# Kernel tuning notes

Measured on AMD Instinct MI355X. Metric: run time of the kernel, lower is better.

Reference implementation:

```python
import jax, jax.numpy as jnp
import numpy as np

D_MODEL = 768
N_HEADS = 12
D_HEAD = D_MODEL // N_HEADS

def setup_inputs() -> dict:
    key = jax.random.key(0)
    ks = jax.random.split(key, 5)
    B, T = 2, 4096
    x = jax.random.normal(ks[0], (B, T, D_MODEL), dtype=jnp.float32)
    s_in = 1.0 / np.sqrt(D_MODEL)
    W_qkv = jax.random.normal(ks[1], (D_MODEL, 3 * D_MODEL), dtype=jnp.float32) * s_in
    b_qkv = jnp.zeros((3 * D_MODEL,), dtype=jnp.float32)
    W_proj = jax.random.normal(ks[2], (D_MODEL, D_MODEL), dtype=jnp.float32) * s_in
    b_proj = jnp.zeros((D_MODEL,), dtype=jnp.float32)
    return {"x": x, "W_qkv": W_qkv, "b_qkv": b_qkv, "W_proj": W_proj, "b_proj": b_proj}

def reference(x, W_qkv, b_qkv, W_proj, b_proj):
    B, T, C = x.shape
    qkv = x @ W_qkv + b_qkv                      # [B,T,3C]
    q, k, v = jnp.split(qkv, 3, axis=-1)
    def heads(t):
        return t.reshape(B, T, N_HEADS, D_HEAD).transpose(0, 2, 1, 3)  # [B,H,T,d]
    q, k, v = heads(q), heads(k), heads(v)
    scale = 1.0 / np.sqrt(D_HEAD)
    att = jnp.einsum('bhqd,bhkd->bhqk', q, k) * scale  # [B,H,T,T]
    causal = jnp.tril(jnp.ones((T, T), dtype=bool))
    att = jnp.where(causal[None, None], att, -jnp.inf)
    att = jax.nn.softmax(att, axis=-1)
    y = jnp.einsum('bhqk,bhkd->bhqd', att, v)          # [B,H,T,d]
    y = y.transpose(0, 2, 1, 3).reshape(B, T, C)
    return y @ W_proj + b_proj
```

## Files before the change

### kernel.cpp

```cpp
#include <hip/hip_runtime.h>
#include <hip/hip_bf16.h>

typedef __bf16 bf16_t;
typedef bf16_t bf16x4 __attribute__((ext_vector_type(4)));
typedef bf16_t bf16x8 __attribute__((ext_vector_type(8)));
typedef float  f32x4  __attribute__((ext_vector_type(4)));

#define TSEQ   4096
#define NBATCH 2
#define DMODEL 768
#define NHEADS 12
#define DHEAD  64
#define NTOK   (NBATCH*TSEQ)
#define NQKV   (3*DMODEL)

#define QSCALE 0.18033688011112042f
#define SMAX 24.0f

__device__ __forceinline__ f32x4 mfma16(bf16x8 a, bf16x8 b, f32x4 c) {
  return __builtin_amdgcn_mfma_f32_16x16x32_bf16(a, b, c, 0, 0, 0);
}

__device__ __forceinline__ void glds16(const bf16_t* g, bf16_t* l) {
  __builtin_amdgcn_global_load_lds(
      (const __attribute__((address_space(1))) void*)g,
      (__attribute__((address_space(3))) void*)l, 16, 0, 0);
}
__device__ __forceinline__ void glds16f(const float* g, float* l) {
  __builtin_amdgcn_global_load_lds(
      (const __attribute__((address_space(1))) void*)g,
      (__attribute__((address_space(3))) void*)l, 16, 0, 0);
}

__global__ __launch_bounds__(256) void k_transpose_cvt(
    const float* __restrict__ in, bf16_t* __restrict__ out, int R, int C) {
  __shared__ bf16_t tile[64][66];
  const int c0 = blockIdx.x * 64, r0 = blockIdx.y * 64;
  const int tid = threadIdx.x;
  const int r = tid >> 2, cb = (tid & 3) * 16;
  const float* ip = in + (long)(r0 + r) * C + c0 + cb;
#pragma unroll
  for (int k = 0; k < 16; k += 4) {
    float4 v = *(const float4*)(ip + k);
    tile[r][cb + k + 0] = (bf16_t)v.x;
    tile[r][cb + k + 1] = (bf16_t)v.y;
    tile[r][cb + k + 2] = (bf16_t)v.z;
    tile[r][cb + k + 3] = (bf16_t)v.w;
  }
  __syncthreads();
  const int c = tid >> 2, rb = (tid & 3) * 16;
  bf16_t* op = out + (long)(c0 + c) * R + r0 + rb;
  bf16x8 v0, v1;
#pragma unroll
  for (int i = 0; i < 8; ++i) { v0[i] = tile[rb + i][c]; v1[i] = tile[rb + 8 + i][c]; }
  *(bf16x8*)(op) = v0;
  *(bf16x8*)(op + 8) = v1;
}

__device__ __forceinline__ void gemm_core(
    const bf16_t* __restrict__ A, const bf16_t* __restrict__ Bt,
    int m0, int n0, bf16_t* As, bf16_t* Bs, f32x4 acc[2][8]) {
  const int tid  = threadIdx.x;
  const int wave = tid >> 6;
  const int lane = tid & 63;
  const int quad = lane >> 4;
  const int l16  = lane & 15;
  const int srow = lane >> 2;
  const int scol = (lane & 3) * 8;

  const bf16_t* a0 = A + (long)(m0 + wave * 16 + srow) * DMODEL + scol;
  const bf16_t* b0 = Bt + (long)(n0 + wave * 16 + srow) * DMODEL + scol;

  glds16(a0,               As + wave * 16 * 32);
  glds16(a0 + 64 * DMODEL, As + (64 + wave * 16) * 32);
  glds16(b0,               Bs + wave * 16 * 32);
  glds16(b0 + 64 * DMODEL, Bs + (64 + wave * 16) * 32);
  __syncthreads();

  for (int ks = 0; ks < DMODEL / 32; ++ks) {
    const int p = ks & 1;
    if (ks + 1 < DMODEL / 32) {
      const int k1 = (ks + 1) * 32;
      bf16_t* Asx = (p ? As : As + 128 * 32);
      bf16_t* Bsx = (p ? Bs : Bs + 128 * 32);
      glds16(a0 + k1,               Asx + wave * 16 * 32);
      glds16(a0 + 64 * DMODEL + k1, Asx + (64 + wave * 16) * 32);
      glds16(b0 + k1,               Bsx + wave * 16 * 32);
      glds16(b0 + 64 * DMODEL + k1, Bsx + (64 + wave * 16) * 32);
    }
    const bf16_t* Ap = As + p * (128 * 32);
    const bf16_t* Bp = Bs + p * (128 * 32);

    bf16x8 af0 = *(const bf16x8*)(Ap + (wave * 32 + l16) * 32 + quad * 8);
    bf16x8 af1 = *(const bf16x8*)(Ap + (wave * 32 + 16 + l16) * 32 + quad * 8);
#pragma unroll
    for (int nt = 0; nt < 8; ++nt) {
      bf16x8 bfm = *(const bf16x8*)(Bp + (nt * 16 + l16) * 32 + quad * 8);
      acc[0][nt] = mfma16(af0, bfm, acc[0][nt]);
      acc[1][nt] = mfma16(af1, bfm, acc[1][nt]);
    }
    __syncthreads();
  }
}

__global__ __launch_bounds__(256) void k_gemm_qkv(
    const float* __restrict__ X, const bf16_t* __restrict__ Bt,
    const float* __restrict__ bias,
    bf16_t* __restrict__ Qo, bf16_t* __restrict__ Ko, bf16_t* __restrict__ Vt) {
  __shared__ __align__(16) float  Asf[2 * 128 * 32];
  __shared__ __align__(16) bf16_t Bs[2 * 128 * 32];
  const int wave = threadIdx.x >> 6;
  const int lane = threadIdx.x & 63;
  const int quad = lane >> 4;
  const int l16  = lane & 15;
  const int m0 = blockIdx.x * 128;
  const int n0 = blockIdx.y * 128;

  const int arow = lane >> 3;
  const int achk = (lane & 7) ^ arow;
  const float* x0 = X + (long)(m0 + wave * 8 + arow) * DMODEL + achk * 4;
  const int srow = lane >> 2;
  const int scol = (lane & 3) * 8;
  const bf16_t* b0 = Bt + (long)(n0 + wave * 16 + srow) * DMODEL + scol;

  f32x4 acc[2][8] = {};

#pragma unroll
  for (int i = 0; i < 4; ++i)
    glds16f(x0 + (long)i * 32 * DMODEL, Asf + (i * 32 + wave * 8) * 32);
  glds16(b0,               Bs + wave * 16 * 32);
  glds16(b0 + 64 * DMODEL, Bs + (64 + wave * 16) * 32);
  __syncthreads();

  const int sk = l16 & 7;
  for (int ks = 0; ks < DMODEL / 32; ++ks) {
    const int p = ks & 1;
    if (ks + 1 < DMODEL / 32) {
      const int k1 = (ks + 1) * 32;
      float*  Asx = (p ? Asf : Asf + 128 * 32);
      bf16_t* Bsx = (p ? Bs : Bs + 128 * 32);
#pragma unroll
      for (int i = 0; i < 4; ++i)
        glds16f(x0 + (long)i * 32 * DMODEL + k1, Asx + (i * 32 + wave * 8) * 32);
      glds16(b0 + k1,               Bsx + wave * 16 * 32);
      glds16(b0 + 64 * DMODEL + k1, Bsx + (64 + wave * 16) * 32);
    }
    const float*  Ap = Asf + p * (128 * 32);
    const bf16_t* Bp = Bs + p * (128 * 32);

    const int r0 = wave * 32 + l16, r1 = r0 + 16;
    f32x4 a0lo = *(const f32x4*)(Ap + r0 * 32 + (((2 * quad)     ^ sk) << 2));
    f32x4 a0hi = *(const f32x4*)(Ap + r0 * 32 + (((2 * quad + 1) ^ sk) << 2));
    f32x4 a1lo = *(const f32x4*)(Ap + r1 * 32 + (((2 * quad)     ^ sk) << 2));
    f32x4 a1hi = *(const f32x4*)(Ap + r1 * 32 + (((2 * quad + 1) ^ sk) << 2));
    bf16x8 af0, af1;
#pragma unroll
    for (int j = 0; j < 4; ++j) {
      af0[j] = (bf16_t)a0lo[j]; af0[4 + j] = (bf16_t)a0hi[j];
      af1[j] = (bf16_t)a1lo[j]; af1[4 + j] = (bf16_t)a1hi[j];
    }
#pragma unroll
    for (int nt = 0; nt < 8; ++nt) {
      bf16x8 bfm = *(const bf16x8*)(Bp + (nt * 16 + l16) * 32 + quad * 8);
      acc[0][nt] = mfma16(af0, bfm, acc[0][nt]);
      acc[1][nt] = mfma16(af1, bfm, acc[1][nt]);
    }
    __syncthreads();
  }

#pragma unroll
  for (int s = 0; s < 2; ++s)
#pragma unroll
    for (int nt = 0; nt < 8; ++nt) {
      const int n = n0 + nt * 16 + l16;
      const float bv = bias[n];
      const int mb = m0 + wave * 32 + s * 16 + quad * 4;
      const int b = mb >> 12;
      const int t = mb & 4095;
      if (n < DMODEL) {
        const int h = n >> 6, d = n & 63;
        bf16_t* qp = Qo + (((long)(b * NHEADS + h) * TSEQ + t) << 6) + d;
#pragma unroll
        for (int j = 0; j < 4; ++j)
          qp[(long)j << 6] = (bf16_t)((acc[s][nt][j] + bv) * QSCALE);
      } else if (n < 2 * DMODEL) {
        const int n2 = n - DMODEL, h = n2 >> 6, d = n2 & 63;
        bf16_t* kp = Ko + (((long)(b * NHEADS + h) * TSEQ + t) << 6) + d;
#pragma unroll
        for (int j = 0; j < 4; ++j)
          kp[(long)j << 6] = (bf16_t)(acc[s][nt][j] + bv);
      } else {
        const int n2 = n - 2 * DMODEL, h = n2 >> 6, d = n2 & 63;
        bf16x4 v;
#pragma unroll
        for (int j = 0; j < 4; ++j) v[j] = (bf16_t)(acc[s][nt][j] + bv);
        *(bf16x4*)(Vt + ((long)(b * NHEADS + h) * DHEAD + d) * TSEQ + t) = v;
      }
    }
}

__global__ __launch_bounds__(256) void k_gemm_proj(
    const bf16_t* __restrict__ A, const bf16_t* __restrict__ Bt,
    const float* __restrict__ bias, float* __restrict__ out) {
  __shared__ __align__(16) bf16_t As[2 * 128 * 32];
  __shared__ __align__(16) bf16_t Bs[2 * 128 * 32];
  const int wave = threadIdx.x >> 6;
  const int lane = threadIdx.x & 63;
  const int quad = lane >> 4;
  const int l16  = lane & 15;
  const int m0 = blockIdx.x * 128;
  const int n0 = blockIdx.y * 128;

  f32x4 acc[2][8] = {};
  gemm_core(A, Bt, m0, n0, As, Bs, acc);

#pragma unroll
  for (int s = 0; s < 2; ++s)
#pragma unroll
    for (int nt = 0; nt < 8; ++nt) {
      const int n = n0 + nt * 16 + l16;
      const float bv = bias[n];
#pragma unroll
      for (int j = 0; j < 4; ++j) {
        const int m = m0 + wave * 32 + s * 16 + quad * 4 + j;
        out[(long)m * DMODEL + n] = acc[s][nt][j] + bv;
      }
    }
}

__global__ __launch_bounds__(256, 2) void k_attn(
    const bf16_t* __restrict__ Q, const bf16_t* __restrict__ K,
    const bf16_t* __restrict__ Vt,
    bf16_t* __restrict__ P0, bf16_t* __restrict__ P1,
    float* __restrict__ L0, float* __restrict__ L1) {
  __shared__ __align__(16) bf16_t kbuf[2][64 * 64];
  __shared__ __align__(16) bf16_t vbuf[2][64 * 64];
  const int wave = threadIdx.x >> 6;
  const int lane = threadIdx.x & 63;
  const int quad = lane >> 4;
  const int l16  = lane & 15;
  const int bh = blockIdx.x;
  const int qt = 15 - (blockIdx.y >> 1);
  const int sp = blockIdx.y & 1;
  const int half = 2 * qt + 2;
  const int c0 = sp ? half : 0;
  const int niter = half;
  bf16_t* Pp = sp ? P1 : P0;
  float*  Lp = sp ? L1 : L0;

  const bf16_t* Qh = Q + ((long)bh * TSEQ << 6);
  const bf16_t* Kh = K + ((long)bh * TSEQ << 6);
  const bf16_t* Vh = Vt + (long)bh * DHEAD * TSEQ;

  const int qbase = qt * 256 + wave * 64;

  bf16x8 qf[4][2];
#pragma unroll
  for (int s = 0; s < 4; ++s) {
    const bf16_t* qrow = Qh + ((long)(qbase + s * 16 + l16) << 6);
    qf[s][0] = *(const bf16x8*)(qrow + quad * 8);
    qf[s][1] = *(const bf16x8*)(qrow + 32 + quad * 8);
  }

  f32x4 acc[4][4] = {};
  float lS[4] = {0.f, 0.f, 0.f, 0.f};
  const f32x4 minit = {-SMAX, -SMAX, -SMAX, -SMAX};

  const int kperm = ((l16 >> 2) << 3) + (l16 & 3);
  const int swl = l16 & 7;
  const int srow = lane >> 3;
  const int cV = (lane & 7) ^ (srow & 7);
  const int cK0 = (lane & 7) ^ (srow & 3);
  const int cK1 = cK0 ^ 4;
  const int r0a = wave * 16, r0b = wave * 16 + 8;

  {
    const int k00 = c0 << 6;
    glds16(Kh + ((long)(k00 + r0a + srow) << 6) + cK0 * 8, &kbuf[0][r0a * 64]);
    glds16(Kh + ((long)(k00 + r0b + srow) << 6) + cK1 * 8, &kbuf[0][r0b * 64]);
    glds16(Vh + (long)(r0a + srow) * TSEQ + k00 + cV * 8,  &vbuf[0][r0a * 64]);
    glds16(Vh + (long)(r0b + srow) * TSEQ + k00 + cV * 8,  &vbuf[0][r0b * 64]);
  }
  __syncthreads();

  for (int ci = 0; ci < niter; ++ci) {
    const int p = ci & 1;
    const int k0 = (c0 + ci) << 6;
    if (ci + 1 < niter) {
      const int k1 = k0 + 64;
      glds16(Kh + ((long)(k1 + r0a + srow) << 6) + cK0 * 8, &kbuf[1 - p][r0a * 64]);
      glds16(Kh + ((long)(k1 + r0b + srow) << 6) + cK1 * 8, &kbuf[1 - p][r0b * 64]);
      glds16(Vh + (long)(r0a + srow) * TSEQ + k1 + cV * 8,  &vbuf[1 - p][r0a * 64]);
      glds16(Vh + (long)(r0b + srow) * TSEQ + k1 + cV * 8,  &vbuf[1 - p][r0b * 64]);
    }
    const bf16_t* kb = kbuf[p];
    const bf16_t* vb = vbuf[p];

#pragma unroll
    for (int g = 0; g < 2; ++g) {
      const int rw0 = (g * 32 + kperm) * 64;
      const int rw1 = (g * 32 + 4 + kperm) * 64;
      bf16x8 kf00 = *(const bf16x8*)(kb + rw0 + ((quad ^ swl) << 3));
      bf16x8 kf01 = *(const bf16x8*)(kb + rw0 + (((quad + 4) ^ swl) << 3));
      bf16x8 kf10 = *(const bf16x8*)(kb + rw1 + ((quad ^ swl) << 3));
      bf16x8 kf11 = *(const bf16x8*)(kb + rw1 + (((quad + 4) ^ swl) << 3));
      const bool domask = (k0 + g * 32 + 31 > qbase);

      bf16x8 pf[4];
#pragma unroll
      for (int s = 0; s < 4; ++s) {
        f32x4 st0 = minit, st1 = minit;
        st0 = mfma16(kf00, qf[s][0], st0);
        st0 = mfma16(kf01, qf[s][1], st0);
        st1 = mfma16(kf10, qf[s][0], st1);
        st1 = mfma16(kf11, qf[s][1], st1);
        if (domask) {
          const int qS = qbase + s * 16 + l16;
          const int kb0 = k0 + g * 32 + quad * 8;
#pragma unroll
          for (int j = 0; j < 4; ++j) {
            if (kb0 + j > qS)     st0[j] = -1e30f;
            if (kb0 + 4 + j > qS) st1[j] = -1e30f;
          }
        }
        float rs = 0.f;
#pragma unroll
        for (int j = 0; j < 4; ++j) {
          float e0 = __builtin_amdgcn_exp2f(st0[j]);
          float e1 = __builtin_amdgcn_exp2f(st1[j]);
          rs += e0 + e1;
          pf[s][j]     = (bf16_t)e0;
          pf[s][4 + j] = (bf16_t)e1;
        }
        lS[s] += rs;
      }
#pragma unroll
      for (int dt = 0; dt < 4; ++dt) {
        const int row = dt * 16 + l16;
        bf16x8 vf = *(const bf16x8*)(vb + row * 64 + ((((g << 2) + quad) ^ swl) << 3));
#pragma unroll
        for (int s = 0; s < 4; ++s)
          acc[s][dt] = mfma16(vf, pf[s], acc[s][dt]);
      }
    }
    __syncthreads();
  }

#pragma unroll
  for (int s = 0; s < 4; ++s) {
    lS[s] += __shfl_xor(lS[s], 16);
    lS[s] += __shfl_xor(lS[s], 32);
  }
#pragma unroll
  for (int s = 0; s < 4; ++s) {
    const int qS = qbase + s * 16 + l16;
    bf16_t* prow = Pp + (((long)bh * TSEQ + qS) << 6);
#pragma unroll
    for (int dt = 0; dt < 4; ++dt)
#pragma unroll
      for (int j = 0; j < 4; ++j)
        prow[dt * 16 + quad * 4 + j] = (bf16_t)acc[s][dt][j];
    if (quad == 0) Lp[(long)bh * TSEQ + qS] = lS[s];
  }
}

__global__ __launch_bounds__(256) void k_combine(
    const bf16_t* __restrict__ P0, const bf16_t* __restrict__ P1,
    const float* __restrict__ L0, const float* __restrict__ L1,
    bf16_t* __restrict__ Y) {
  const int f = (blockIdx.x * 256 + threadIdx.x) * 8;
  const int tok = f / DMODEL;
  const int c = f - tok * DMODEL;
  const int b = tok >> 12, q = tok & 4095;
  const int h = c >> 6, d0 = c & 63;
  const long bhq = (long)(b * NHEADS + h) * TSEQ + q;
  const long pidx = (bhq << 6) + d0;
  bf16x8 o0 = *(const bf16x8*)(P0 + pidx);
  bf16x8 o1 = *(const bf16x8*)(P1 + pidx);
  const float inv = 1.f / (L0[bhq] + L1[bhq]);
  bf16x8 r;
#pragma unroll
  for (int i = 0; i < 8; ++i) r[i] = (bf16_t)(((float)o0[i] + (float)o1[i]) * inv);
  *(bf16x8*)(Y + f) = r;
}

extern "C" void kernel_launch(void* const* d_in, const int* in_sizes, int n_in,
                              void* d_out, int out_size, void* d_ws, size_t ws_size,
                              hipStream_t stream) {
  (void)in_sizes; (void)n_in; (void)out_size; (void)ws_size;
  const float* x     = (const float*)d_in[0];
  const float* Wqkv  = (const float*)d_in[1];
  const float* bqkv  = (const float*)d_in[2];
  const float* Wproj = (const float*)d_in[3];
  const float* bproj = (const float*)d_in[4];
  float* out = (float*)d_out;

  char* ws = (char*)d_ws;
  bf16_t* wqkv_t  = (bf16_t*)ws; ws += (long)NQKV * DMODEL * 2;
  bf16_t* wproj_t = (bf16_t*)ws; ws += (long)DMODEL * DMODEL * 2;
  bf16_t* Qb      = (bf16_t*)ws; ws += (long)NTOK * DMODEL * 2;
  bf16_t* Kb      = (bf16_t*)ws; ws += (long)NTOK * DMODEL * 2;
  bf16_t* Vtb     = (bf16_t*)ws; ws += (long)NTOK * DMODEL * 2;
  bf16_t* Sb      = (bf16_t*)ws; ws += (long)NTOK * DMODEL * 2;
  bf16_t* P0b     = (bf16_t*)ws; ws += (long)NTOK * DMODEL * 2;
  bf16_t* P1b     = (bf16_t*)ws; ws += (long)NTOK * DMODEL * 2;
  float*  L0b     = (float*)ws;  ws += (long)NHEADS * NBATCH * TSEQ * 4;
  float*  L1b     = (float*)ws;  ws += (long)NHEADS * NBATCH * TSEQ * 4;

  k_transpose_cvt<<<dim3(NQKV / 64, DMODEL / 64), 256, 0, stream>>>(Wqkv, wqkv_t, DMODEL, NQKV);
  k_transpose_cvt<<<dim3(DMODEL / 64, DMODEL / 64), 256, 0, stream>>>(Wproj, wproj_t, DMODEL, DMODEL);

  k_gemm_qkv<<<dim3(NTOK / 128, NQKV / 128), 256, 0, stream>>>(x, wqkv_t, bqkv, Qb, Kb, Vtb);
  k_attn<<<dim3(NBATCH * NHEADS, 32), 256, 0, stream>>>(Qb, Kb, Vtb, P0b, P1b, L0b, L1b);
  k_combine<<<(NTOK * DMODEL) / (256 * 8), 256, 0, stream>>>(P0b, P1b, L0b, L1b, Sb);
  k_gemm_proj<<<dim3(NTOK / 128, DMODEL / 128), 256, 0, stream>>>(Sb, wproj_t, bproj, out);
}
```

Measured before the change: 233.2 us.

## Merge weight transposes, halve proj GEMM M tile, widen attention KV chunks

```diff
diff --git a/kernel.cpp b/kernel.cpp
--- a/kernel.cpp
+++ b/kernel.cpp
@@ -32,10 +32,16 @@
       (__attribute__((address_space(3))) void*)l, 16, 0, 0);
 }
 
-__global__ __launch_bounds__(256) void k_transpose_cvt(
-    const float* __restrict__ in, bf16_t* __restrict__ out, int R, int C) {
+__global__ __launch_bounds__(256) void k_transpose_cvt2(
+    const float* __restrict__ W1, bf16_t* __restrict__ O1,
+    const float* __restrict__ W2, bf16_t* __restrict__ O2) {
   __shared__ bf16_t tile[64][66];
-  const int c0 = blockIdx.x * 64, r0 = blockIdx.y * 64;
+  int t = blockIdx.x;
+  const float* in; bf16_t* out; int R, C, c0, r0;
+  if (t < 432) { in = W1; out = O1; R = DMODEL; C = NQKV;
+                 c0 = (t % 36) * 64; r0 = (t / 36) * 64; }
+  else { t -= 432; in = W2; out = O2; R = DMODEL; C = DMODEL;
+         c0 = (t % 12) * 64; r0 = (t / 12) * 64; }
   const int tid = threadIdx.x;
   const int r = tid >> 2, cb = (tid & 3) * 16;
   const float* ip = in + (long)(r0 + r) * C + c0 + cb;
@@ -55,52 +61,6 @@
   for (int i = 0; i < 8; ++i) { v0[i] = tile[rb + i][c]; v1[i] = tile[rb + 8 + i][c]; }
   *(bf16x8*)(op) = v0;
   *(bf16x8*)(op + 8) = v1;
-}
-
-__device__ __forceinline__ void gemm_core(
-    const bf16_t* __restrict__ A, const bf16_t* __restrict__ Bt,
-    int m0, int n0, bf16_t* As, bf16_t* Bs, f32x4 acc[2][8]) {
-  const int tid  = threadIdx.x;
-  const int wave = tid >> 6;
-  const int lane = tid & 63;
-  const int quad = lane >> 4;
-  const int l16  = lane & 15;
-  const int srow = lane >> 2;
-  const int scol = (lane & 3) * 8;
-
-  const bf16_t* a0 = A + (long)(m0 + wave * 16 + srow) * DMODEL + scol;
-  const bf16_t* b0 = Bt + (long)(n0 + wave * 16 + srow) * DMODEL + scol;
-
-  glds16(a0,               As + wave * 16 * 32);
-  glds16(a0 + 64 * DMODEL, As + (64 + wave * 16) * 32);
-  glds16(b0,               Bs + wave * 16 * 32);
-  glds16(b0 + 64 * DMODEL, Bs + (64 + wave * 16) * 32);
-  __syncthreads();
-
-  for (int ks = 0; ks < DMODEL / 32; ++ks) {
-    const int p = ks & 1;
-    if (ks + 1 < DMODEL / 32) {
-      const int k1 = (ks + 1) * 32;
-      bf16_t* Asx = (p ? As : As + 128 * 32);
-      bf16_t* Bsx = (p ? Bs : Bs + 128 * 32);
-      glds16(a0 + k1,               Asx + wave * 16 * 32);
-      glds16(a0 + 64 * DMODEL + k1, Asx + (64 + wave * 16) * 32);
-      glds16(b0 + k1,               Bsx + wave * 16 * 32);
-      glds16(b0 + 64 * DMODEL + k1, Bsx + (64 + wave * 16) * 32);
-    }
-    const bf16_t* Ap = As + p * (128 * 32);
-    const bf16_t* Bp = Bs + p * (128 * 32);
-
-    bf16x8 af0 = *(const bf16x8*)(Ap + (wave * 32 + l16) * 32 + quad * 8);
-    bf16x8 af1 = *(const bf16x8*)(Ap + (wave * 32 + 16 + l16) * 32 + quad * 8);
-#pragma unroll
-    for (int nt = 0; nt < 8; ++nt) {
-      bf16x8 bfm = *(const bf16x8*)(Bp + (nt * 16 + l16) * 32 + quad * 8);
-      acc[0][nt] = mfma16(af0, bfm, acc[0][nt]);
-      acc[1][nt] = mfma16(af1, bfm, acc[1][nt]);
-    }
-    __syncthreads();
-  }
 }
 
 __global__ __launch_bounds__(256) void k_gemm_qkv(
@@ -202,30 +162,59 @@
 __global__ __launch_bounds__(256) void k_gemm_proj(
     const bf16_t* __restrict__ A, const bf16_t* __restrict__ Bt,
     const float* __restrict__ bias, float* __restrict__ out) {
-  __shared__ __align__(16) bf16_t As[2 * 128 * 32];
+  __shared__ __align__(16) bf16_t As[2 * 64 * 32];
   __shared__ __align__(16) bf16_t Bs[2 * 128 * 32];
   const int wave = threadIdx.x >> 6;
   const int lane = threadIdx.x & 63;
   const int quad = lane >> 4;
   const int l16  = lane & 15;
-  const int m0 = blockIdx.x * 128;
+  const int m0 = blockIdx.x * 64;
   const int n0 = blockIdx.y * 128;
 
-  f32x4 acc[2][8] = {};
-  gemm_core(A, Bt, m0, n0, As, Bs, acc);
-
-#pragma unroll
-  for (int s = 0; s < 2; ++s)
+  const int srow = lane >> 2;
+  const int scol = (lane & 3) * 8;
+  const bf16_t* a0 = A + (long)(m0 + wave * 16 + srow) * DMODEL + scol;
+  const bf16_t* b0 = Bt + (long)(n0 + wave * 16 + srow) * DMODEL + scol;
+
+  f32x4 acc[8] = {};
+
+  glds16(a0,               As + wave * 16 * 32);
+  glds16(b0,               Bs + wave * 16 * 32);
+  glds16(b0 + 64 * DMODEL, Bs + (64 + wave * 16) * 32);
+  __syncthreads();
+
+  for (int ks = 0; ks < DMODEL / 32; ++ks) {
+    const int p = ks & 1;
+    if (ks + 1 < DMODEL / 32) {
+      const int k1 = (ks + 1) * 32;
+      bf16_t* Asx = (p ? As : As + 64 * 32);
+      bf16_t* Bsx = (p ? Bs : Bs + 128 * 32);
+      glds16(a0 + k1,               Asx + wave * 16 * 32);
+      glds16(b0 + k1,               Bsx + wave * 16 * 32);
+      glds16(b0 + 64 * DMODEL + k1, Bsx + (64 + wave * 16) * 32);
+    }
+    const bf16_t* Ap = As + p * (64 * 32);
+    const bf16_t* Bp = Bs + p * (128 * 32);
+
+    bf16x8 af = *(const bf16x8*)(Ap + (wave * 16 + l16) * 32 + quad * 8);
 #pragma unroll
     for (int nt = 0; nt < 8; ++nt) {
-      const int n = n0 + nt * 16 + l16;
-      const float bv = bias[n];
-#pragma unroll
-      for (int j = 0; j < 4; ++j) {
-        const int m = m0 + wave * 32 + s * 16 + quad * 4 + j;
-        out[(long)m * DMODEL + n] = acc[s][nt][j] + bv;
-      }
-    }
+      bf16x8 bfm = *(const bf16x8*)(Bp + (nt * 16 + l16) * 32 + quad * 8);
+      acc[nt] = mfma16(af, bfm, acc[nt]);
+    }
+    __syncthreads();
+  }
+
+#pragma unroll
+  for (int nt = 0; nt < 8; ++nt) {
+    const int n = n0 + nt * 16 + l16;
+    const float bv = bias[n];
+#pragma unroll
+    for (int j = 0; j < 4; ++j) {
+      const int m = m0 + wave * 16 + quad * 4 + j;
+      out[(long)m * DMODEL + n] = acc[nt][j] + bv;
+    }
+  }
 }
 
 __global__ __launch_bounds__(256, 2) void k_attn(
@@ -233,8 +222,8 @@
     const bf16_t* __restrict__ Vt,
     bf16_t* __restrict__ P0, bf16_t* __restrict__ P1,
     float* __restrict__ L0, float* __restrict__ L1) {
-  __shared__ __align__(16) bf16_t kbuf[2][64 * 64];
-  __shared__ __align__(16) bf16_t vbuf[2][64 * 64];
+  __shared__ __align__(16) bf16_t kbuf[2][128 * 64];
+  __shared__ __align__(16) bf16_t vbuf[2][64 * 128];
   const int wave = threadIdx.x >> 6;
   const int lane = threadIdx.x & 63;
   const int quad = lane >> 4;
@@ -242,9 +231,8 @@
   const int bh = blockIdx.x;
   const int qt = 15 - (blockIdx.y >> 1);
   const int sp = blockIdx.y & 1;
-  const int half = 2 * qt + 2;
-  const int c0 = sp ? half : 0;
-  const int niter = half;
+  const int niter = qt + 1;
+  const int c0 = sp ? niter : 0;
   bf16_t* Pp = sp ? P1 : P0;
   float*  Lp = sp ? L1 : L0;
 
@@ -268,36 +256,40 @@
 
   const int kperm = ((l16 >> 2) << 3) + (l16 & 3);
   const int swl = l16 & 7;
-  const int srow = lane >> 3;
-  const int cV = (lane & 7) ^ (srow & 7);
-  const int cK0 = (lane & 7) ^ (srow & 3);
-  const int cK1 = cK0 ^ 4;
-  const int r0a = wave * 16, r0b = wave * 16 + 8;
-
-  {
-    const int k00 = c0 << 6;
-    glds16(Kh + ((long)(k00 + r0a + srow) << 6) + cK0 * 8, &kbuf[0][r0a * 64]);
-    glds16(Kh + ((long)(k00 + r0b + srow) << 6) + cK1 * 8, &kbuf[0][r0b * 64]);
-    glds16(Vh + (long)(r0a + srow) * TSEQ + k00 + cV * 8,  &vbuf[0][r0a * 64]);
-    glds16(Vh + (long)(r0b + srow) * TSEQ + k00 + cV * 8,  &vbuf[0][r0b * 64]);
-  }
+  const int srow8  = lane >> 3;
+  const int ck_lo  = (lane & 7) ^ (srow8 & 3);
+  const int srow16 = lane >> 4;
+
+#define STAGE_CHUNK(buf, kbase)                                              \
+  {                                                                          \
+    _Pragma("unroll")                                                        \
+    for (int i = 0; i < 4; ++i) {                                            \
+      const int kr = wave * 32 + 8 * i;                                      \
+      const int cK = ck_lo ^ ((i & 1) << 2);                                 \
+      glds16(Kh + ((long)((kbase) + kr + srow8) << 6) + cK * 8,              \
+             &kbuf[buf][kr * 64]);                                           \
+    }                                                                        \
+    _Pragma("unroll")                                                        \
+    for (int i = 0; i < 4; ++i) {                                            \
+      const int vr = wave * 16 + 4 * i;                                      \
+      const int cV = (lane & 15) ^ ((vr + srow16) & 7);                      \
+      glds16(Vh + (long)(vr + srow16) * TSEQ + (kbase) + cV * 8,             \
+             &vbuf[buf][vr * 128]);                                          \
+    }                                                                        \
+  }
+
+  STAGE_CHUNK(0, c0 << 7)
   __syncthreads();
 
   for (int ci = 0; ci < niter; ++ci) {
     const int p = ci & 1;
-    const int k0 = (c0 + ci) << 6;
-    if (ci + 1 < niter) {
-      const int k1 = k0 + 64;
-      glds16(Kh + ((long)(k1 + r0a + srow) << 6) + cK0 * 8, &kbuf[1 - p][r0a * 64]);
-      glds16(Kh + ((long)(k1 + r0b + srow) << 6) + cK1 * 8, &kbuf[1 - p][r0b * 64]);
-      glds16(Vh + (long)(r0a + srow) * TSEQ + k1 + cV * 8,  &vbuf[1 - p][r0a * 64]);
-      glds16(Vh + (long)(r0b + srow) * TSEQ + k1 + cV * 8,  &vbuf[1 - p][r0b * 64]);
-    }
+    const int k0 = (c0 + ci) << 7;
+    if (ci + 1 < niter) STAGE_CHUNK(1 - p, k0 + 128)
     const bf16_t* kb = kbuf[p];
     const bf16_t* vb = vbuf[p];
 
 #pragma unroll
-    for (int g = 0; g < 2; ++g) {
+    for (int g = 0; g < 4; ++g) {
       const int rw0 = (g * 32 + kperm) * 64;
       const int rw1 = (g * 32 + 4 + kperm) * 64;
       bf16x8 kf00 = *(const bf16x8*)(kb + rw0 + ((quad ^ swl) << 3));
@@ -337,7 +329,7 @@
 #pragma unroll
       for (int dt = 0; dt < 4; ++dt) {
         const int row = dt * 16 + l16;
-        bf16x8 vf = *(const bf16x8*)(vb + row * 64 + ((((g << 2) + quad) ^ swl) << 3));
+        bf16x8 vf = *(const bf16x8*)(vb + row * 128 + ((((g << 2) + quad) ^ swl) << 3));
 #pragma unroll
         for (int s = 0; s < 4; ++s)
           acc[s][dt] = mfma16(vf, pf[s], acc[s][dt]);
@@ -407,11 +399,9 @@
   float*  L0b     = (float*)ws;  ws += (long)NHEADS * NBATCH * TSEQ * 4;
   float*  L1b     = (float*)ws;  ws += (long)NHEADS * NBATCH * TSEQ * 4;
 
-  k_transpose_cvt<<<dim3(NQKV / 64, DMODEL / 64), 256, 0, stream>>>(Wqkv, wqkv_t, DMODEL, NQKV);
-  k_transpose_cvt<<<dim3(DMODEL / 64, DMODEL / 64), 256, 0, stream>>>(Wproj, wproj_t, DMODEL, DMODEL);
-
+  k_transpose_cvt2<<<576, 256, 0, stream>>>(Wqkv, wqkv_t, Wproj, wproj_t);
   k_gemm_qkv<<<dim3(NTOK / 128, NQKV / 128), 256, 0, stream>>>(x, wqkv_t, bqkv, Qb, Kb, Vtb);
   k_attn<<<dim3(NBATCH * NHEADS, 32), 256, 0, stream>>>(Qb, Kb, Vtb, P0b, P1b, L0b, L1b);
   k_combine<<<(NTOK * DMODEL) / (256 * 8), 256, 0, stream>>>(P0b, P1b, L0b, L1b, Sb);
-  k_gemm_proj<<<dim3(NTOK / 128, DMODEL / 128), 256, 0, stream>>>(Sb, wproj_t, bproj, out);
-}
+  k_gemm_proj<<<dim3(NTOK / 64, DMODEL / 128), 256, 0, stream>>>(Sb, wproj_t, bproj, out);
+}
```

Result: slower. 316.0 us (+35.5%).
